# Kernel tuning notes

Hardware: AMD Instinct MI355X
Metric: run time of the kernel (lower is better)

Reference implementation:

```python
import jax, jax.numpy as jnp
import numpy as np

D_MODEL = 1024
N_HEADS = 16
D_KEYS = D_MODEL // N_HEADS


def setup_inputs() -> dict:
    key = jax.random.key(0)
    ks = jax.random.split(key, 11)
    B, L, S = 2, 2048, 2048
    inp = {
        "queries": jax.random.normal(ks[0], (B, L, D_MODEL), dtype=jnp.float32),
        "keys": jax.random.normal(ks[1], (B, S, D_MODEL), dtype=jnp.float32),
        "values": jax.random.normal(ks[2], (B, S, D_MODEL), dtype=jnp.float32),
        # Linear params, scaled like torch default init (~U(-1/sqrt(D), 1/sqrt(D)))
        "Wq": jax.random.normal(ks[3], (D_MODEL, D_MODEL), dtype=jnp.float32) / np.sqrt(D_MODEL),
        "bq": jax.random.normal(ks[4], (D_MODEL,), dtype=jnp.float32) / np.sqrt(D_MODEL),
        "Wk": jax.random.normal(ks[5], (D_MODEL, D_MODEL), dtype=jnp.float32) / np.sqrt(D_MODEL),
        "bk": jax.random.normal(ks[6], (D_MODEL,), dtype=jnp.float32) / np.sqrt(D_MODEL),
        "Wv": jax.random.normal(ks[7], (D_MODEL, D_MODEL), dtype=jnp.float32) / np.sqrt(D_MODEL),
        "bv": jax.random.normal(ks[8], (D_MODEL,), dtype=jnp.float32) / np.sqrt(D_MODEL),
        "Wo": jax.random.normal(ks[9], (D_MODEL, D_MODEL), dtype=jnp.float32) / np.sqrt(D_MODEL),
        "bo": jax.random.normal(ks[10], (D_MODEL,), dtype=jnp.float32) / np.sqrt(D_MODEL),
    }
    return inp


def reference(queries, keys, values, Wq, bq, Wk, bk, Wv, bv, Wo, bo):
    B, L, _ = queries.shape
    S = keys.shape[1]
    H, E = N_HEADS, D_KEYS
    scale = E ** (-0.5)
    q = (queries @ Wq.T + bq).reshape(B, L, H, E)
    k = (keys @ Wk.T + bk).reshape(B, S, H, E)
    v = (values @ Wv.T + bv).reshape(B, S, H, E)
    scores = jnp.einsum('blhe,bshe->bhls', q, k)
    attn = jax.nn.softmax(scores * scale, axis=-1)  # dropout = identity in eval
    out = jnp.einsum('bhls,bshe->blhe', attn, v).reshape(B, L, H * E)
    return out @ Wo.T + bo
```

## Files before the change

kernel.cpp:

```cpp
#include <hip/hip_runtime.h>

typedef unsigned short u16;
typedef unsigned int u32;
typedef __attribute__((ext_vector_type(8))) short short8;
typedef __attribute__((ext_vector_type(4))) short s16x4;
typedef __attribute__((ext_vector_type(4))) float f32x4;
typedef __attribute__((ext_vector_type(16))) float f32x16;

#define DEVI __device__ __forceinline__

#define LSEQ 2048
#define DMODEL 1024
#define NH 16
#define EHD 64

#define QSCALE 0.18033688011112042f

#if __has_builtin(__builtin_amdgcn_exp2f)
#define EXP2(x) __builtin_amdgcn_exp2f(x)
#else
#define EXP2(x) exp2f(x)
#endif

DEVI u16 f2b(float f) {
    u32 u = __float_as_uint(f);
    return (u16)((u + 0x7FFFu + ((u >> 16) & 1u)) >> 16);
}

DEVI u32 cvtpk(float lo, float hi) {
    u32 r;
    asm("v_cvt_pk_bf16_f32 %0, %1, %2" : "=v"(r) : "v"(lo), "v"(hi));
    return r;
}

DEVI void swap32(u32& a, u32& b) {
    asm("v_permlane32_swap_b32 %0, %1" : "+v"(a), "+v"(b));
}

DEVI short8 mk8(u32 a0, u32 a1, u32 a2, u32 a3) {
    union { u32 u[4]; short8 s; } x;
    x.u[0] = a0; x.u[1] = a1; x.u[2] = a2; x.u[3] = a3;
    return x.s;
}

DEVI void async_cp16(const void* g, void* l) {
    __builtin_amdgcn_global_load_lds((const __attribute__((address_space(1))) u32*)g,
                                     (__attribute__((address_space(3))) u32*)l, 16, 0, 0);
}

DEVI short8 lds_swz(const u16* base, int row, int colb) {
    int off = (row << 7) + (colb ^ ((row & 7) << 4));
    return *(const short8*)((const char*)base + off);
}

__global__ __launch_bounds__(256) void cvt_all(const float* __restrict__ q,
                                               const float* __restrict__ k,
                                               const float* __restrict__ v,
                                               const float* __restrict__ wq,
                                               const float* __restrict__ wk,
                                               const float* __restrict__ wv,
                                               const float* __restrict__ wo,
                                               u16* __restrict__ dst) {
    const size_t NX8 = (size_t)2 * LSEQ * DMODEL / 8;
    const size_t NW8 = (size_t)DMODEL * DMODEL / 8;
    int bid = blockIdx.x;
    const float* src;
    size_t base;
    int rel;
    if (bid < 2048)      { src = q;  base = 0;             rel = bid; }
    else if (bid < 4096) { src = k;  base = NX8;           rel = bid - 2048; }
    else if (bid < 6144) { src = v;  base = 2 * NX8;       rel = bid - 4096; }
    else if (bid < 6656) { src = wq; base = 3 * NX8;             rel = bid - 6144; }
    else if (bid < 7168) { src = wk; base = 3 * NX8 + NW8;       rel = bid - 6656; }
    else if (bid < 7680) { src = wv; base = 3 * NX8 + 2 * NW8;   rel = bid - 7168; }
    else                 { src = wo; base = 3 * NX8 + 3 * NW8;   rel = bid - 7680; }
    size_t i = (size_t)rel * 256 + threadIdx.x;
    const float4* p = (const float4*)(src + i * 8);
    float4 a = p[0], c = p[1];
    short8 o;
    o[0] = (short)f2b(a.x); o[1] = (short)f2b(a.y);
    o[2] = (short)f2b(a.z); o[3] = (short)f2b(a.w);
    o[4] = (short)f2b(c.x); o[5] = (short)f2b(c.y);
    o[6] = (short)f2b(c.z); o[7] = (short)f2b(c.w);
    *(short8*)(dst + (base + i) * 8) = o;
}

__global__ __launch_bounds__(512, 1) void gemm_qkv(const u16* __restrict__ X,
                                                   const u16* __restrict__ W3,
                                                   const float* __restrict__ bq,
                                                   const float* __restrict__ bk,
                                                   const float* __restrict__ bv,
                                                   u16* __restrict__ Qp,
                                                   u16* __restrict__ Kp,
                                                   u16* __restrict__ Vt) {
    __shared__ __align__(16) u16 As[2][16384];
    __shared__ __align__(16) u16 Bs[2][16384];
    const int tid = threadIdx.x;
    const int lane = tid & 63;
    const int w = tid >> 6;
    const int lr = lane & 15, lk = lane >> 4;
    const int wm = w >> 2, wn = w & 3;
    const int bid = blockIdx.x;
    const int xcd = bid & 7, rr = bid >> 3;
    const int rb = (xcd * 2 + rr / 12) * 256;
    const int cb = (rr % 12) * 256;
    const int K = DMODEL;
    const int seg = cb >> 10;
    const u16* A = X + (size_t)seg * ((size_t)2 * LSEQ * DMODEL);

    f32x4 acc[8][4] = {};

    const int srow = tid >> 3;
    const int sslot = tid & 7;
    size_t abase[4], bbase[4];
#pragma unroll
    for (int i = 0; i < 4; i++) {
        int row = i * 64 + srow;
        int swz = ((sslot ^ (row & 7)) * 8);
        abase[i] = (size_t)(rb + row) * K + swz;
        bbase[i] = (size_t)(cb + row) * K + swz;
    }

#define QS_A(bb, kk)                                                         \
    do {                                                                     \
        _Pragma("unroll") for (int i = 0; i < 4; i++)                        \
            async_cp16(A + abase[i] + (kk), &As[bb][(i * 512 + tid) * 8]);   \
    } while (0)
#define QS_B(bb, kk)                                                         \
    do {                                                                     \
        _Pragma("unroll") for (int i = 0; i < 4; i++)                        \
            async_cp16(W3 + bbase[i] + (kk), &Bs[bb][(i * 512 + tid) * 8]);  \
    } while (0)

#define QKV_MM(ac_, mt)                                                                   \
    do {                                                                                  \
        short8 a0 = lds_swz(ac_, wm * 128 + (mt) * 16 + lr, lk * 16);                     \
        short8 a1 = lds_swz(ac_, wm * 128 + (mt) * 16 + lr, 64 + lk * 16);                \
        short8 a2 = lds_swz(ac_, wm * 128 + (mt) * 16 + 16 + lr, lk * 16);                \
        short8 a3 = lds_swz(ac_, wm * 128 + (mt) * 16 + 16 + lr, 64 + lk * 16);           \
        __builtin_amdgcn_s_setprio(1);                                                    \
        _Pragma("unroll") for (int n = 0; n < 4; n++) {                                   \
            acc[mt][n] = __builtin_amdgcn_mfma_f32_16x16x32_bf16(a0, bf[n][0], acc[mt][n], 0, 0, 0);       \
            acc[mt][n] = __builtin_amdgcn_mfma_f32_16x16x32_bf16(a1, bf[n][1], acc[mt][n], 0, 0, 0);       \
            acc[(mt) + 1][n] = __builtin_amdgcn_mfma_f32_16x16x32_bf16(a2, bf[n][0], acc[(mt) + 1][n], 0, 0, 0); \
            acc[(mt) + 1][n] = __builtin_amdgcn_mfma_f32_16x16x32_bf16(a3, bf[n][1], acc[(mt) + 1][n], 0, 0, 0); \
        }                                                                                 \
        __builtin_amdgcn_s_setprio(0);                                                    \
    } while (0)

    QS_A(0, 0);
    QS_B(0, 0);
    asm volatile("s_waitcnt vmcnt(0)" ::: "memory");
    __builtin_amdgcn_s_barrier();

    int cur = 0;
    for (int t = 0; t < 16; ++t) {
        const u16* ac = &As[cur][0];
        const u16* bc = &Bs[cur][0];
        const bool st = (t + 1 < 16);
        const int kk = (t + 1) * 64;

        if (st) QS_A(cur ^ 1, kk);
        short8 bf[4][2];
#pragma unroll
        for (int n = 0; n < 4; n++) {
            bf[n][0] = lds_swz(bc, wn * 64 + n * 16 + lr, lk * 16);
            bf[n][1] = lds_swz(bc, wn * 64 + n * 16 + lr, 64 + lk * 16);
        }
        QKV_MM(ac, 0);
        if (st) QS_B(cur ^ 1, kk);
        QKV_MM(ac, 2);
        QKV_MM(ac, 4);
        QKV_MM(ac, 6);

        asm volatile("s_waitcnt vmcnt(0)" ::: "memory");
        __builtin_amdgcn_s_barrier();
        cur ^= 1;
    }

    const float* bp = seg == 0 ? bq : (seg == 1 ? bk : bv);
    const float sc = seg == 0 ? QSCALE : 1.0f;

#pragma unroll
    for (int n = 0; n < 4; n++) {
        int col = cb + wn * 64 + n * 16 + lr;
        int c2 = col & 1023;
        float bvv = bp[c2];
#pragma unroll
        for (int m = 0; m < 8; m++) {
            int row0 = rb + wm * 128 + m * 16 + lk * 4;
            if (seg == 2) {
                s16x4 pk4;
#pragma unroll
                for (int r = 0; r < 4; r++) pk4[r] = (short)f2b(acc[m][n][r] + bvv);
                size_t idx = (((size_t)(row0 >> 11) * NH + (c2 >> 6)) * EHD + (c2 & 63)) * LSEQ +
                             (row0 & (LSEQ - 1));
                *(s16x4*)(Vt + idx) = pk4;
            } else {
                u16* dst = seg == 0 ? Qp : Kp;
#pragma unroll
                for (int r = 0; r < 4; r++)
                    dst[(size_t)(row0 + r) * DMODEL + c2] = f2b((acc[m][n][r] + bvv) * sc);
            }
        }
    }
}

__global__ __launch_bounds__(256) void gemm_out(const u16* __restrict__ A,
                                                const u16* __restrict__ B,
                                                const float* __restrict__ bias,
                                                float* __restrict__ C) {
    __shared__ __align__(16) u16 As[3][4096];
    __shared__ __align__(16) u16 Bs[3][2048];
    const int tid = threadIdx.x;
    const int lane = tid & 63, w = tid >> 6;
    const int lr = lane & 15, lk = lane >> 4;
    const int wr = w >> 1, wc = w & 1;
    const int bid = blockIdx.x;
    const int xcd = bid & 7, rr = bid >> 3;
    const int rb = (xcd * 4 + rr / 16) * 128;
    const int cb = (rr % 16) * 64;
    const int K = DMODEL, N = DMODEL;

    f32x4 acc[4][2] = {};

    const int arow = lane >> 2;
    const int acol = (lane & 3) * 8;

#define OUT_STAGE(bb, kk)                                                           \
    do {                                                                            \
        _Pragma("unroll") for (int c2 = 0; c2 < 2; ++c2) {                          \
            int c = w * 2 + c2;                                                     \
            async_cp16(A + (size_t)(rb + c * 16 + arow) * K + (kk) + acol,          \
                       &As[bb][c * 512]);                                           \
        }                                                                           \
        async_cp16(B + (size_t)(cb + w * 16 + arow) * K + (kk) + acol,              \
                   &Bs[bb][w * 512]);                                               \
    } while (0)

#define OUT_ITER(bc, bs, tt)                                                          \
    do {                                                                              \
        if ((tt) + 2 < 32) OUT_STAGE(bs, ((tt) + 2) * 32);                            \
        short8 af[4], bfr[2];                                                         \
        _Pragma("unroll") for (int m = 0; m < 4; m++)                                 \
            af[m] = *(const short8*)(&As[bc][(wr * 64 + m * 16 + lr) * 32 + lk * 8]); \
        _Pragma("unroll") for (int n = 0; n < 2; n++)                                 \
            bfr[n] = *(const short8*)(&Bs[bc][(wc * 32 + n * 16 + lr) * 32 + lk * 8]); \
        __builtin_amdgcn_s_setprio(1);                                                \
        _Pragma("unroll") for (int m = 0; m < 4; m++)                                 \
            _Pragma("unroll") for (int n = 0; n < 2; n++)                             \
                acc[m][n] =                                                           \
                    __builtin_amdgcn_mfma_f32_16x16x32_bf16(af[m], bfr[n], acc[m][n], 0, 0, 0); \
        __builtin_amdgcn_s_setprio(0);                                                \
        if ((tt) + 2 < 32) asm volatile("s_waitcnt vmcnt(3)" ::: "memory");           \
        else               asm volatile("s_waitcnt vmcnt(0)" ::: "memory");           \
        __builtin_amdgcn_s_barrier();                                                 \
    } while (0)

    OUT_STAGE(0, 0);
    OUT_STAGE(1, 32);
    asm volatile("s_waitcnt vmcnt(3)" ::: "memory");
    __builtin_amdgcn_s_barrier();

    for (int tb = 0; tb < 30; tb += 3) {
        OUT_ITER(0, 2, tb);
        OUT_ITER(1, 0, tb + 1);
        OUT_ITER(2, 1, tb + 2);
    }
    OUT_ITER(0, 2, 30);
    OUT_ITER(1, 0, 31);

#pragma unroll
    for (int n = 0; n < 2; n++) {
        int col = cb + wc * 32 + n * 16 + lr;
        float bv = bias[col];
#pragma unroll
        for (int m = 0; m < 4; m++) {
            int row0 = rb + wr * 64 + m * 16 + lk * 4;
#pragma unroll
            for (int r = 0; r < 4; r++)
                C[(size_t)(row0 + r) * N + col] = acc[m][n][r] + bv;
        }
    }
}

__global__ __launch_bounds__(512, 1) void attn_kernel(const u16* __restrict__ Q,
                                                      const u16* __restrict__ Kp,
                                                      const u16* __restrict__ Vtb,
                                                      u16* __restrict__ Hid) {
    const int bid = blockIdx.x;
    const int j = bid >> 3;
    const int bh = (bid & 7) + 8 * (j >> 3);
    const int q0 = (j & 7) * 256;
    const int b = bh >> 4, h = bh & 15;
    const int tid = threadIdx.x, lane = tid & 63, w = tid >> 6;
    const int l31 = lane & 31, hi = lane >> 5;
    const int qb = q0 + w * 32;

    __shared__ __align__(16) u16 Ks[2][16384];
    __shared__ __align__(16) u16 Vs[2][4][4096];

    short8 qf[4];
#pragma unroll
    for (int eg = 0; eg < 4; eg++)
        qf[eg] = *(const short8*)(Q + (size_t)(b * LSEQ + qb + l31) * DMODEL + h * EHD +
                                  eg * 16 + hi * 8);

    const int trow = tid >> 3;
    const int slot = tid & 7;
    const int swz8 = ((slot ^ (trow & 7)) * 8);
    size_t kbase[4], vbase[4];
#pragma unroll
    for (int jj = 0; jj < 4; jj++) {
        kbase[jj] = (size_t)(b * LSEQ + jj * 64 + trow) * DMODEL + h * EHD + swz8;
        vbase[jj] = ((size_t)bh * EHD + trow) * LSEQ + jj * 64 + swz8;
    }

#define ATTN_STAGE(bb, s0v)                                                              \
    do {                                                                                 \
        _Pragma("unroll") for (int jj = 0; jj < 4; jj++)                                 \
            async_cp16(Kp + kbase[jj] + (size_t)(s0v)*DMODEL,                            \
                       &Ks[bb][jj * 4096 + w * 512]);                                    \
        _Pragma("unroll") for (int jj = 0; jj < 4; jj++)                                 \
            async_cp16(Vtb + vbase[jj] + (s0v), &Vs[bb][jj][w * 512]);                   \
    } while (0)

    f32x16 o0 = (f32x16)0.f, o1 = (f32x16)0.f, lsum = (f32x16)0.f;
    const u32 one2 = 0x3F803F80u;
    const short8 ones = mk8(one2, one2, one2, one2);

    ATTN_STAGE(0, 0);
    asm volatile("s_waitcnt vmcnt(0)" ::: "memory");
    __syncthreads();

    int cur = 0;
    for (int t = 0; t < LSEQ / 256; ++t) {
        if (t + 1 < LSEQ / 256) ATTN_STAGE(cur ^ 1, (t + 1) * 256);

#pragma unroll
        for (int hf = 0; hf < 4; hf++) {
            f32x16 s0 = (f32x16)0.f, s1 = (f32x16)0.f;
            __builtin_amdgcn_s_setprio(1);
#pragma unroll
            for (int eg = 0; eg < 4; eg++) {
                short8 kf0 = lds_swz(&Ks[cur][0], hf * 64 + l31, eg * 32 + hi * 16);
                short8 kf1 = lds_swz(&Ks[cur][0], hf * 64 + 32 + l31, eg * 32 + hi * 16);
                s0 = __builtin_amdgcn_mfma_f32_32x32x16_bf16(kf0, qf[eg], s0, 0, 0, 0);
                s1 = __builtin_amdgcn_mfma_f32_32x32x16_bf16(kf1, qf[eg], s1, 0, 0, 0);
            }
            __builtin_amdgcn_s_setprio(0);

#pragma unroll
            for (int r = 0; r < 16; r++) {
                s0[r] = EXP2(s0[r]);
                s1[r] = EXP2(s1[r]);
            }

            short8 paf[4];
#pragma unroll
            for (int kc = 0; kc < 4; kc++) {
                int ro = (kc & 1) * 8;
                u32 u0, u1, u2, u3;
                if (kc < 2) {
                    u0 = cvtpk(s0[ro + 0], s0[ro + 1]); u1 = cvtpk(s0[ro + 2], s0[ro + 3]);
                    u2 = cvtpk(s0[ro + 4], s0[ro + 5]); u3 = cvtpk(s0[ro + 6], s0[ro + 7]);
                } else {
                    u0 = cvtpk(s1[ro + 0], s1[ro + 1]); u1 = cvtpk(s1[ro + 2], s1[ro + 3]);
                    u2 = cvtpk(s1[ro + 4], s1[ro + 5]); u3 = cvtpk(s1[ro + 6], s1[ro + 7]);
                }
                swap32(u0, u2);
                swap32(u1, u3);
                paf[kc] = mk8(u0, u1, u2, u3);
            }

            __builtin_amdgcn_s_setprio(1);
#pragma unroll
            for (int kc = 0; kc < 4; kc++) {
                short8 vf0 = lds_swz(&Vs[cur][hf][0], l31, kc * 32 + hi * 16);
                short8 vf1 = lds_swz(&Vs[cur][hf][0], 32 + l31, kc * 32 + hi * 16);
                o0 = __builtin_amdgcn_mfma_f32_32x32x16_bf16(paf[kc], vf0, o0, 0, 0, 0);
                o1 = __builtin_amdgcn_mfma_f32_32x32x16_bf16(paf[kc], vf1, o1, 0, 0, 0);
                lsum = __builtin_amdgcn_mfma_f32_32x32x16_bf16(paf[kc], ones, lsum, 0, 0, 0);
            }
            __builtin_amdgcn_s_setprio(0);
        }

        asm volatile("s_waitcnt vmcnt(0)" ::: "memory");
        __syncthreads();
        cur ^= 1;
    }

#pragma unroll
    for (int r = 0; r < 16; r++) {
        float li = 1.0f / lsum[r];
        int qrow = qb + (r & 3) + 8 * (r >> 2) + 4 * hi;
        size_t base = (size_t)(b * LSEQ + qrow) * DMODEL + h * EHD;
        Hid[base + l31] = f2b(o0[r] * li);
        Hid[base + 32 + l31] = f2b(o1[r] * li);
    }
}

extern "C" void kernel_launch(void* const* d_in, const int* in_sizes, int n_in,
                              void* d_out, int out_size, void* d_ws, size_t ws_size,
                              hipStream_t stream) {
    const float* queries = (const float*)d_in[0];
    const float* keys    = (const float*)d_in[1];
    const float* values  = (const float*)d_in[2];
    const float* Wq = (const float*)d_in[3];
    const float* bq = (const float*)d_in[4];
    const float* Wk = (const float*)d_in[5];
    const float* bk = (const float*)d_in[6];
    const float* Wv = (const float*)d_in[7];
    const float* bv = (const float*)d_in[8];
    const float* Wo = (const float*)d_in[9];
    const float* bo = (const float*)d_in[10];
    float* out = (float*)d_out;

    const size_t NX = (size_t)2 * LSEQ * DMODEL;
    const size_t NW = (size_t)DMODEL * DMODEL;

    u16* p = (u16*)d_ws;
    u16* Xq = p;  p += NX;
    u16* Xk = p;  p += NX;
    u16* Xv = p;  p += NX;
    u16* Wqb = p; p += NW;
    u16* Wkb = p; p += NW;
    u16* Wvb = p; p += NW;
    u16* Wob = p; p += NW;
    u16* Qp = p;  p += NX;
    u16* Kp = p;  p += NX;
    u16* Vt = p;  p += NX;
    u16* Hid = p; p += NX;
    (void)Xk; (void)Xv; (void)Wkb; (void)Wvb;

    cvt_all<<<8192, 256, 0, stream>>>(queries, keys, values, Wq, Wk, Wv, Wo, Xq);

    gemm_qkv<<<192, 512, 0, stream>>>(Xq, Wqb, bq, bk, bv, Qp, Kp, Vt);

    attn_kernel<<<256, 512, 0, stream>>>(Qp, Kp, Vt, Hid);

    gemm_out<<<512, 256, 0, stream>>>(Hid, Wob, bo, out);
}
```

Baseline: 116.0 us.

## Fuse activation fp32-to-bf16 conversion into QKV GEMM A-tile loads

The separate conversion pass over queries, keys and values is removed. The QKV GEMM now reads fp32 activations straight into registers, packs them to bf16 and writes them into swizzled LDS, overlapped with the MFMA work. The conversion kernel now handles only the four weight matrices. This drops a full write and re-read of the bf16 activation copies. In exchange, A-tile loads go through registers instead of async global-to-LDS copies, the GEMM reads twice the A bytes, and VGPR pressure rises.

```diff
diff --git a/kernel.cpp b/kernel.cpp
--- a/kernel.cpp
+++ b/kernel.cpp
@@ -53,27 +53,15 @@
     return *(const short8*)((const char*)base + off);
 }
 
-__global__ __launch_bounds__(256) void cvt_all(const float* __restrict__ q,
-                                               const float* __restrict__ k,
-                                               const float* __restrict__ v,
-                                               const float* __restrict__ wq,
-                                               const float* __restrict__ wk,
-                                               const float* __restrict__ wv,
-                                               const float* __restrict__ wo,
-                                               u16* __restrict__ dst) {
-    const size_t NX8 = (size_t)2 * LSEQ * DMODEL / 8;
-    const size_t NW8 = (size_t)DMODEL * DMODEL / 8;
+__global__ __launch_bounds__(256) void cvt_w(const float* __restrict__ wq,
+                                             const float* __restrict__ wk,
+                                             const float* __restrict__ wv,
+                                             const float* __restrict__ wo,
+                                             u16* __restrict__ dst) {
     int bid = blockIdx.x;
-    const float* src;
-    size_t base;
-    int rel;
-    if (bid < 2048)      { src = q;  base = 0;             rel = bid; }
-    else if (bid < 4096) { src = k;  base = NX8;           rel = bid - 2048; }
-    else if (bid < 6144) { src = v;  base = 2 * NX8;       rel = bid - 4096; }
-    else if (bid < 6656) { src = wq; base = 3 * NX8;             rel = bid - 6144; }
-    else if (bid < 7168) { src = wk; base = 3 * NX8 + NW8;       rel = bid - 6656; }
-    else if (bid < 7680) { src = wv; base = 3 * NX8 + 2 * NW8;   rel = bid - 7168; }
-    else                 { src = wo; base = 3 * NX8 + 3 * NW8;   rel = bid - 7680; }
+    const float* src = bid < 512 ? wq : (bid < 1024 ? wk : (bid < 1536 ? wv : wo));
+    int rel = bid & 511;
+    size_t base = (size_t)(bid >> 9) * ((size_t)DMODEL * DMODEL);
     size_t i = (size_t)rel * 256 + threadIdx.x;
     const float4* p = (const float4*)(src + i * 8);
     float4 a = p[0], c = p[1];
@@ -82,10 +70,12 @@
     o[2] = (short)f2b(a.z); o[3] = (short)f2b(a.w);
     o[4] = (short)f2b(c.x); o[5] = (short)f2b(c.y);
     o[6] = (short)f2b(c.z); o[7] = (short)f2b(c.w);
-    *(short8*)(dst + (base + i) * 8) = o;
-}
-
-__global__ __launch_bounds__(512, 1) void gemm_qkv(const u16* __restrict__ X,
+    *(short8*)(dst + base + i * 8) = o;
+}
+
+__global__ __launch_bounds__(512, 1) void gemm_qkv(const float* __restrict__ Xq,
+                                                   const float* __restrict__ Xk,
+                                                   const float* __restrict__ Xv,
                                                    const u16* __restrict__ W3,
                                                    const float* __restrict__ bq,
                                                    const float* __restrict__ bk,
@@ -106,30 +96,44 @@
     const int cb = (rr % 12) * 256;
     const int K = DMODEL;
     const int seg = cb >> 10;
-    const u16* A = X + (size_t)seg * ((size_t)2 * LSEQ * DMODEL);
+    const float* A = seg == 0 ? Xq : (seg == 1 ? Xk : Xv);
 
     f32x4 acc[8][4] = {};
+
+    const int arw = tid >> 1;
+    const int akh = (tid & 1) * 32;
+    const float* Abase = A + (size_t)(rb + arw) * K + akh;
 
     const int srow = tid >> 3;
     const int sslot = tid & 7;
-    size_t abase[4], bbase[4];
+    size_t bbase[4];
 #pragma unroll
     for (int i = 0; i < 4; i++) {
         int row = i * 64 + srow;
-        int swz = ((sslot ^ (row & 7)) * 8);
-        abase[i] = (size_t)(rb + row) * K + swz;
-        bbase[i] = (size_t)(cb + row) * K + swz;
-    }
-
-#define QS_A(bb, kk)                                                         \
-    do {                                                                     \
-        _Pragma("unroll") for (int i = 0; i < 4; i++)                        \
-            async_cp16(A + abase[i] + (kk), &As[bb][(i * 512 + tid) * 8]);   \
-    } while (0)
+        bbase[i] = (size_t)(cb + row) * K + ((sslot ^ (row & 7)) * 8);
+    }
+
 #define QS_B(bb, kk)                                                         \
     do {                                                                     \
         _Pragma("unroll") for (int i = 0; i < 4; i++)                        \
             async_cp16(W3 + bbase[i] + (kk), &Bs[bb][(i * 512 + tid) * 8]);  \
+    } while (0)
+
+#define QKV_LDA(kk)                                                          \
+    do {                                                                     \
+        _Pragma("unroll") for (int i = 0; i < 8; i++)                        \
+            av[i] = *(const float4*)(Abase + (kk) + i * 4);                  \
+    } while (0)
+
+#define QKV_STA(bb)                                                                     \
+    do {                                                                                \
+        _Pragma("unroll") for (int j = 0; j < 4; j++) {                                 \
+            int sIdx = ((tid & 1) * 4 + j) ^ (arw & 7);                                 \
+            *(short8*)(&As[bb][arw * 64 + sIdx * 8]) =                                  \
+                mk8(cvtpk(av[2 * j][0], av[2 * j][1]), cvtpk(av[2 * j][2], av[2 * j][3]), \
+                    cvtpk(av[2 * j + 1][0], av[2 * j + 1][1]),                          \
+                    cvtpk(av[2 * j + 1][2], av[2 * j + 1][3]));                         \
+        }                                                                               \
     } while (0)
 
 #define QKV_MM(ac_, mt)                                                                   \
@@ -148,10 +152,14 @@
         __builtin_amdgcn_s_setprio(0);                                                    \
     } while (0)
 
-    QS_A(0, 0);
-    QS_B(0, 0);
-    asm volatile("s_waitcnt vmcnt(0)" ::: "memory");
-    __builtin_amdgcn_s_barrier();
+    {
+        float4 av[8];
+        QKV_LDA(0);
+        QS_B(0, 0);
+        QKV_STA(0);
+        asm volatile("s_waitcnt vmcnt(0) lgkmcnt(0)" ::: "memory");
+        __builtin_amdgcn_s_barrier();
+    }
 
     int cur = 0;
     for (int t = 0; t < 16; ++t) {
@@ -160,7 +168,8 @@
         const bool st = (t + 1 < 16);
         const int kk = (t + 1) * 64;
 
-        if (st) QS_A(cur ^ 1, kk);
+        float4 av[8];
+        if (st) QKV_LDA(kk);
         short8 bf[4][2];
 #pragma unroll
         for (int n = 0; n < 4; n++) {
@@ -171,9 +180,10 @@
         if (st) QS_B(cur ^ 1, kk);
         QKV_MM(ac, 2);
         QKV_MM(ac, 4);
+        if (st) QKV_STA(cur ^ 1);
         QKV_MM(ac, 6);
 
-        asm volatile("s_waitcnt vmcnt(0)" ::: "memory");
+        asm volatile("s_waitcnt vmcnt(0) lgkmcnt(0)" ::: "memory");
         __builtin_amdgcn_s_barrier();
         cur ^= 1;
     }
@@ -420,9 +430,6 @@
     const size_t NW = (size_t)DMODEL * DMODEL;
 
     u16* p = (u16*)d_ws;
-    u16* Xq = p;  p += NX;
-    u16* Xk = p;  p += NX;
-    u16* Xv = p;  p += NX;
     u16* Wqb = p; p += NW;
     u16* Wkb = p; p += NW;
     u16* Wvb = p; p += NW;
@@ -431,11 +438,11 @@
     u16* Kp = p;  p += NX;
     u16* Vt = p;  p += NX;
     u16* Hid = p; p += NX;
-    (void)Xk; (void)Xv; (void)Wkb; (void)Wvb;
-
-    cvt_all<<<8192, 256, 0, stream>>>(queries, keys, values, Wq, Wk, Wv, Wo, Xq);
-
-    gemm_qkv<<<192, 512, 0, stream>>>(Xq, Wqb, bq, bk, bv, Qp, Kp, Vt);
+    (void)Wkb; (void)Wvb;
+
+    cvt_w<<<2048, 256, 0, stream>>>(Wq, Wk, Wv, Wo, Wqb);
+
+    gemm_qkv<<<192, 512, 0, stream>>>(queries, keys, values, Wqb, bq, bk, bv, Qp, Kp, Vt);
 
     attn_kernel<<<256, 512, 0, stream>>>(Qp, Kp, Vt, Hid);
 
```

New measurement: 128.5 us. 1.11x slower.

## Software-pipeline QK^T of the next subtile with softmax and PV of the current

Applied to the files above, without the earlier changes.

Restructures the inner attention loop into a ping-pong schedule with two score buffers. The QK^T MFMAs for subtile hf+1 are issued before the exp/convert and PV MFMAs of subtile hf. The aim is to overlap the VALU exp2 and pack work with matrix-core work and hide MFMA latency. The cost is higher register pressure from holding an extra pair of f32x16 accumulators, which could reduce occupancy or cause spills.

```diff
diff --git a/kernel.cpp b/kernel.cpp
--- a/kernel.cpp
+++ b/kernel.cpp
@@ -329,6 +329,51 @@
     const u32 one2 = 0x3F803F80u;
     const short8 ones = mk8(one2, one2, one2, one2);
 
+#define QKT(kcp_, hf, d0, d1)                                                            \
+    do {                                                                                 \
+        __builtin_amdgcn_s_setprio(1);                                                   \
+        _Pragma("unroll") for (int eg = 0; eg < 4; eg++) {                               \
+            short8 kf0 = lds_swz(kcp_, (hf) * 64 + l31, eg * 32 + hi * 16);              \
+            short8 kf1 = lds_swz(kcp_, (hf) * 64 + 32 + l31, eg * 32 + hi * 16);         \
+            d0 = __builtin_amdgcn_mfma_f32_32x32x16_bf16(kf0, qf[eg], d0, 0, 0, 0);      \
+            d1 = __builtin_amdgcn_mfma_f32_32x32x16_bf16(kf1, qf[eg], d1, 0, 0, 0);      \
+        }                                                                                \
+        __builtin_amdgcn_s_setprio(0);                                                   \
+    } while (0)
+
+#define SMPV(s0v, s1v, hf)                                                               \
+    do {                                                                                 \
+        _Pragma("unroll") for (int r = 0; r < 16; r++) {                                 \
+            s0v[r] = EXP2(s0v[r]);                                                       \
+            s1v[r] = EXP2(s1v[r]);                                                       \
+        }                                                                                \
+        short8 paf[4];                                                                   \
+        _Pragma("unroll") for (int kc = 0; kc < 4; kc++) {                               \
+            int ro = (kc & 1) * 8;                                                       \
+            u32 u0, u1, u2, u3;                                                          \
+            if (kc < 2) {                                                                \
+                u0 = cvtpk(s0v[ro + 0], s0v[ro + 1]); u1 = cvtpk(s0v[ro + 2], s0v[ro + 3]); \
+                u2 = cvtpk(s0v[ro + 4], s0v[ro + 5]); u3 = cvtpk(s0v[ro + 6], s0v[ro + 7]); \
+            } else {                                                                     \
+                u0 = cvtpk(s1v[ro + 0], s1v[ro + 1]); u1 = cvtpk(s1v[ro + 2], s1v[ro + 3]); \
+                u2 = cvtpk(s1v[ro + 4], s1v[ro + 5]); u3 = cvtpk(s1v[ro + 6], s1v[ro + 7]); \
+            }                                                                            \
+            swap32(u0, u2);                                                              \
+            swap32(u1, u3);                                                              \
+            paf[kc] = mk8(u0, u1, u2, u3);                                               \
+        }                                                                                \
+        const u16* vsp = &Vs[cur][hf][0];                                                \
+        __builtin_amdgcn_s_setprio(1);                                                   \
+        _Pragma("unroll") for (int kc = 0; kc < 4; kc++) {                               \
+            short8 vf0 = lds_swz(vsp, l31, kc * 32 + hi * 16);                           \
+            short8 vf1 = lds_swz(vsp, 32 + l31, kc * 32 + hi * 16);                      \
+            o0 = __builtin_amdgcn_mfma_f32_32x32x16_bf16(paf[kc], vf0, o0, 0, 0, 0);     \
+            o1 = __builtin_amdgcn_mfma_f32_32x32x16_bf16(paf[kc], vf1, o1, 0, 0, 0);     \
+            lsum = __builtin_amdgcn_mfma_f32_32x32x16_bf16(paf[kc], ones, lsum, 0, 0, 0); \
+        }                                                                                \
+        __builtin_amdgcn_s_setprio(0);                                                   \
+    } while (0)
+
     ATTN_STAGE(0, 0);
     asm volatile("s_waitcnt vmcnt(0)" ::: "memory");
     __syncthreads();
@@ -336,54 +381,20 @@
     int cur = 0;
     for (int t = 0; t < LSEQ / 256; ++t) {
         if (t + 1 < LSEQ / 256) ATTN_STAGE(cur ^ 1, (t + 1) * 256);
-
-#pragma unroll
-        for (int hf = 0; hf < 4; hf++) {
-            f32x16 s0 = (f32x16)0.f, s1 = (f32x16)0.f;
-            __builtin_amdgcn_s_setprio(1);
-#pragma unroll
-            for (int eg = 0; eg < 4; eg++) {
-                short8 kf0 = lds_swz(&Ks[cur][0], hf * 64 + l31, eg * 32 + hi * 16);
-                short8 kf1 = lds_swz(&Ks[cur][0], hf * 64 + 32 + l31, eg * 32 + hi * 16);
-                s0 = __builtin_amdgcn_mfma_f32_32x32x16_bf16(kf0, qf[eg], s0, 0, 0, 0);
-                s1 = __builtin_amdgcn_mfma_f32_32x32x16_bf16(kf1, qf[eg], s1, 0, 0, 0);
-            }
-            __builtin_amdgcn_s_setprio(0);
-
-#pragma unroll
-            for (int r = 0; r < 16; r++) {
-                s0[r] = EXP2(s0[r]);
-                s1[r] = EXP2(s1[r]);
-            }
-
-            short8 paf[4];
-#pragma unroll
-            for (int kc = 0; kc < 4; kc++) {
-                int ro = (kc & 1) * 8;
-                u32 u0, u1, u2, u3;
-                if (kc < 2) {
-                    u0 = cvtpk(s0[ro + 0], s0[ro + 1]); u1 = cvtpk(s0[ro + 2], s0[ro + 3]);
-                    u2 = cvtpk(s0[ro + 4], s0[ro + 5]); u3 = cvtpk(s0[ro + 6], s0[ro + 7]);
-                } else {
-                    u0 = cvtpk(s1[ro + 0], s1[ro + 1]); u1 = cvtpk(s1[ro + 2], s1[ro + 3]);
-                    u2 = cvtpk(s1[ro + 4], s1[ro + 5]); u3 = cvtpk(s1[ro + 6], s1[ro + 7]);
-                }
-                swap32(u0, u2);
-                swap32(u1, u3);
-                paf[kc] = mk8(u0, u1, u2, u3);
-            }
-
-            __builtin_amdgcn_s_setprio(1);
-#pragma unroll
-            for (int kc = 0; kc < 4; kc++) {
-                short8 vf0 = lds_swz(&Vs[cur][hf][0], l31, kc * 32 + hi * 16);
-                short8 vf1 = lds_swz(&Vs[cur][hf][0], 32 + l31, kc * 32 + hi * 16);
-                o0 = __builtin_amdgcn_mfma_f32_32x32x16_bf16(paf[kc], vf0, o0, 0, 0, 0);
-                o1 = __builtin_amdgcn_mfma_f32_32x32x16_bf16(paf[kc], vf1, o1, 0, 0, 0);
-                lsum = __builtin_amdgcn_mfma_f32_32x32x16_bf16(paf[kc], ones, lsum, 0, 0, 0);
-            }
-            __builtin_amdgcn_s_setprio(0);
-        }
+        const u16* kcp = &Ks[cur][0];
+
+        f32x16 sE0 = (f32x16)0.f, sE1 = (f32x16)0.f;
+        f32x16 sO0 = (f32x16)0.f, sO1 = (f32x16)0.f;
+        QKT(kcp, 0, sE0, sE1);
+        QKT(kcp, 1, sO0, sO1);
+        SMPV(sE0, sE1, 0);
+        sE0 = (f32x16)0.f; sE1 = (f32x16)0.f;
+        QKT(kcp, 2, sE0, sE1);
+        SMPV(sO0, sO1, 1);
+        sO0 = (f32x16)0.f; sO1 = (f32x16)0.f;
+        QKT(kcp, 3, sO0, sO1);
+        SMPV(sE0, sE1, 2);
+        SMPV(sO0, sO1, 3);
 
         asm volatile("s_waitcnt vmcnt(0)" ::: "memory");
         __syncthreads();
```

Result: no change. 116.2 us (+0.2%).

## Restructure output GEMM to 256x64 tiles with swizzled LDS and K=64 stages

Applied to the files above, without the earlier changes.

The output projection GEMM moves from 128x64 tiles with 256 threads and a 3-stage K=32 pipeline to 256x64 tiles with 512 threads and a 2-stage K=64 double buffer. LDS uses an XOR swizzle read through lds_swz, and each wave computes a 32x64 sub-tile. The aim is better reuse of each loaded B tile, fewer barriers per K, and fewer bank conflicts. In exchange it launches half as many blocks, pipelines less deeply, and waits on vmcnt(0) every iteration.

```diff
diff --git a/kernel.cpp b/kernel.cpp
--- a/kernel.cpp
+++ b/kernel.cpp
@@ -206,77 +206,88 @@
     }
 }
 
-__global__ __launch_bounds__(256) void gemm_out(const u16* __restrict__ A,
-                                                const u16* __restrict__ B,
-                                                const float* __restrict__ bias,
-                                                float* __restrict__ C) {
-    __shared__ __align__(16) u16 As[3][4096];
-    __shared__ __align__(16) u16 Bs[3][2048];
+__global__ __launch_bounds__(512, 1) void gemm_out(const u16* __restrict__ A,
+                                                   const u16* __restrict__ B,
+                                                   const float* __restrict__ bias,
+                                                   float* __restrict__ C) {
+    __shared__ __align__(16) u16 As[2][16384];
+    __shared__ __align__(16) u16 Bs[2][4096];
     const int tid = threadIdx.x;
-    const int lane = tid & 63, w = tid >> 6;
+    const int lane = tid & 63;
+    const int w = tid >> 6;
     const int lr = lane & 15, lk = lane >> 4;
-    const int wr = w >> 1, wc = w & 1;
     const int bid = blockIdx.x;
     const int xcd = bid & 7, rr = bid >> 3;
-    const int rb = (xcd * 4 + rr / 16) * 128;
+    const int rb = (xcd * 2 + rr / 16) * 256;
     const int cb = (rr % 16) * 64;
     const int K = DMODEL, N = DMODEL;
 
-    f32x4 acc[4][2] = {};
-
-    const int arow = lane >> 2;
-    const int acol = (lane & 3) * 8;
-
-#define OUT_STAGE(bb, kk)                                                           \
-    do {                                                                            \
-        _Pragma("unroll") for (int c2 = 0; c2 < 2; ++c2) {                          \
-            int c = w * 2 + c2;                                                     \
-            async_cp16(A + (size_t)(rb + c * 16 + arow) * K + (kk) + acol,          \
-                       &As[bb][c * 512]);                                           \
-        }                                                                           \
-        async_cp16(B + (size_t)(cb + w * 16 + arow) * K + (kk) + acol,              \
-                   &Bs[bb][w * 512]);                                               \
-    } while (0)
-
-#define OUT_ITER(bc, bs, tt)                                                          \
-    do {                                                                              \
-        if ((tt) + 2 < 32) OUT_STAGE(bs, ((tt) + 2) * 32);                            \
-        short8 af[4], bfr[2];                                                         \
-        _Pragma("unroll") for (int m = 0; m < 4; m++)                                 \
-            af[m] = *(const short8*)(&As[bc][(wr * 64 + m * 16 + lr) * 32 + lk * 8]); \
-        _Pragma("unroll") for (int n = 0; n < 2; n++)                                 \
-            bfr[n] = *(const short8*)(&Bs[bc][(wc * 32 + n * 16 + lr) * 32 + lk * 8]); \
-        __builtin_amdgcn_s_setprio(1);                                                \
-        _Pragma("unroll") for (int m = 0; m < 4; m++)                                 \
-            _Pragma("unroll") for (int n = 0; n < 2; n++)                             \
-                acc[m][n] =                                                           \
-                    __builtin_amdgcn_mfma_f32_16x16x32_bf16(af[m], bfr[n], acc[m][n], 0, 0, 0); \
-        __builtin_amdgcn_s_setprio(0);                                                \
-        if ((tt) + 2 < 32) asm volatile("s_waitcnt vmcnt(3)" ::: "memory");           \
-        else               asm volatile("s_waitcnt vmcnt(0)" ::: "memory");           \
-        __builtin_amdgcn_s_barrier();                                                 \
-    } while (0)
-
-    OUT_STAGE(0, 0);
-    OUT_STAGE(1, 32);
-    asm volatile("s_waitcnt vmcnt(3)" ::: "memory");
+    f32x4 acc[2][4] = {};
+
+    const int srow = tid >> 3;
+    const int sslot = tid & 7;
+    size_t abase[4];
+#pragma unroll
+    for (int i = 0; i < 4; i++) {
+        int row = i * 64 + srow;
+        abase[i] = (size_t)(rb + row) * K + ((sslot ^ (row & 7)) * 8);
+    }
+    const size_t obbase = (size_t)(cb + srow) * K + ((sslot ^ (srow & 7)) * 8);
+
+#define OS_A(bb, kk)                                                         \
+    do {                                                                     \
+        _Pragma("unroll") for (int i = 0; i < 4; i++)                        \
+            async_cp16(A + abase[i] + (kk), &As[bb][(i * 512 + tid) * 8]);   \
+    } while (0)
+#define OS_B(bb, kk) async_cp16(B + obbase + (kk), &Bs[bb][tid * 8])
+
+#define OUT_MM(ac_, mt)                                                                  \
+    do {                                                                                 \
+        short8 a0 = lds_swz(ac_, w * 32 + (mt) * 16 + lr, lk * 16);                      \
+        short8 a1 = lds_swz(ac_, w * 32 + (mt) * 16 + lr, 64 + lk * 16);                 \
+        __builtin_amdgcn_s_setprio(1);                                                   \
+        _Pragma("unroll") for (int n = 0; n < 4; n++) {                                  \
+            acc[mt][n] = __builtin_amdgcn_mfma_f32_16x16x32_bf16(a0, bf[n][0], acc[mt][n], 0, 0, 0); \
+            acc[mt][n] = __builtin_amdgcn_mfma_f32_16x16x32_bf16(a1, bf[n][1], acc[mt][n], 0, 0, 0); \
+        }                                                                                \
+        __builtin_amdgcn_s_setprio(0);                                                   \
+    } while (0)
+
+    OS_A(0, 0);
+    OS_B(0, 0);
+    asm volatile("s_waitcnt vmcnt(0)" ::: "memory");
     __builtin_amdgcn_s_barrier();
 
-    for (int tb = 0; tb < 30; tb += 3) {
-        OUT_ITER(0, 2, tb);
-        OUT_ITER(1, 0, tb + 1);
-        OUT_ITER(2, 1, tb + 2);
-    }
-    OUT_ITER(0, 2, 30);
-    OUT_ITER(1, 0, 31);
-
-#pragma unroll
-    for (int n = 0; n < 2; n++) {
-        int col = cb + wc * 32 + n * 16 + lr;
+    int cur = 0;
+    for (int t = 0; t < 16; ++t) {
+        const u16* ac = &As[cur][0];
+        const u16* bc = &Bs[cur][0];
+        const bool st = (t + 1 < 16);
+        const int kk = (t + 1) * 64;
+
+        if (st) OS_A(cur ^ 1, kk);
+        short8 bf[4][2];
+#pragma unroll
+        for (int n = 0; n < 4; n++) {
+            bf[n][0] = lds_swz(bc, n * 16 + lr, lk * 16);
+            bf[n][1] = lds_swz(bc, n * 16 + lr, 64 + lk * 16);
+        }
+        OUT_MM(ac, 0);
+        if (st) OS_B(cur ^ 1, kk);
+        OUT_MM(ac, 1);
+
+        asm volatile("s_waitcnt vmcnt(0)" ::: "memory");
+        __builtin_amdgcn_s_barrier();
+        cur ^= 1;
+    }
+
+#pragma unroll
+    for (int n = 0; n < 4; n++) {
+        int col = cb + n * 16 + lr;
         float bv = bias[col];
 #pragma unroll
-        for (int m = 0; m < 4; m++) {
-            int row0 = rb + wr * 64 + m * 16 + lk * 4;
+        for (int m = 0; m < 2; m++) {
+            int row0 = rb + w * 32 + m * 16 + lk * 4;
 #pragma unroll
             for (int r = 0; r < 4; r++)
                 C[(size_t)(row0 + r) * N + col] = acc[m][n][r] + bv;
@@ -439,5 +450,5 @@
 
     attn_kernel<<<256, 512, 0, stream>>>(Qp, Kp, Vt, Hid);
 
-    gemm_out<<<512, 256, 0, stream>>>(Hid, Wob, bo, out);
-}
+    gemm_out<<<256, 512, 0, stream>>>(Hid, Wob, bo, out);
+}
```

After: 116.8 us. No clear change (+0.7%).
